# Kernel optimization log

Hardware: AMD Instinct MI355X
Metric: run time of the kernel (lower is better)

The kernel has to match this reference:

```python
import jax, jax.numpy as jnp
import numpy as np

V, D, H, HR, E, C = 32000, 512, 2048, 512, 8, 16
B, S = 2048, 128
MAX_PATH_LEN = 5
MAX_VISITS = 1
NEG = -1e9


def setup_inputs() -> dict:
    key = jax.random.key(0)
    ks = jax.random.split(key, 16)
    sc = 0.02
    emb = jax.random.normal(ks[0], (V, D), jnp.float32) * sc
    emb = emb.at[0].set(0.0)  # padding_idx = 0
    inp = {
        'input_ids': jax.random.randint(ks[1], (B, S), 0, V, jnp.int32),
        'emb': emb,
        'rW1': jax.random.normal(ks[2], (D, HR), jnp.float32) * sc,
        'rb1': jnp.zeros((HR,), jnp.float32),
        'rW2': jax.random.normal(ks[3], (HR, E + 1), jnp.float32) * sc,
        'rb2': jnp.zeros((E + 1,), jnp.float32),
        'eW1': jax.random.normal(ks[4], (E, D, H), jnp.float32) * sc,
        'eb1': jnp.zeros((E, H), jnp.float32),
        'eW2': jax.random.normal(ks[5], (E, H, D), jnp.float32) * sc,
        'eb2': jnp.zeros((E, D), jnp.float32),
        'etag': jax.random.normal(ks[6], (E, D), jnp.float32) * 0.1,  # specialization_tag
        'cW': jax.random.normal(ks[7], (D, C), jnp.float32) * sc,
        'cb': jnp.zeros((C,), jnp.float32),
    }
    return inp


def _goe_forward(input_ids, emb, rW1, rb1, rW2, rb2, eW1, eb1, eW2, eb2, etag, cW, cb):
    # mean-pooled token embeddings -> [B, D]
    rep = emb[input_ids].mean(axis=1)
    b = rep.shape[0]
    active = jnp.ones((b,), bool)
    visits = jnp.zeros((b, E), jnp.int32)
    final = jnp.zeros_like(rep)
    total_ent = jnp.asarray(0.0, rep.dtype)

    for _ in range(MAX_PATH_LEN):
        # router with visit-count masking
        hr = jax.nn.relu(rep @ rW1 + rb1)
        logits = hr @ rW2 + rb2  # [B, E+1]
        mask = jnp.concatenate([visits >= MAX_VISITS,
                                jnp.zeros((b, 1), bool)], axis=1)
        logits = jnp.where(mask, NEG, logits)
        probs = jax.nn.softmax(logits, axis=1)
        ent_per = -(probs * jnp.log(probs + 1e-9)).sum(axis=1)
        n_act = active.sum()
        step_ent = jnp.where(active, ent_per, 0.0).sum() / jnp.maximum(n_act, 1)
        total_ent = total_ent + jnp.where(n_act > 0, step_ent, 0.0)

        # eval-mode hard argmax decision (index E == terminate)
        decision = jnp.argmax(logits, axis=1)
        terminate = decision == E
        newly_term = active & terminate
        final = jnp.where(newly_term[:, None], rep, final)
        continuing = active & ~terminate
        chosen = jnp.clip(decision, 0, E - 1)

        # dense all-expert MLP, then gather the chosen expert's output
        hh = jax.nn.relu(jnp.einsum('bd,edh->beh', rep, eW1) + eb1)  # [B,E,H]
        out = jnp.einsum('beh,ehd->bed', hh, eW2) + eb2 + etag       # [B,E,D]
        new_rep = jnp.take_along_axis(out, chosen[:, None, None], axis=1)[:, 0, :]

        rep = jnp.where(continuing[:, None], new_rep, rep)
        visits = visits + jax.nn.one_hot(chosen, E, dtype=visits.dtype) \
            * continuing[:, None].astype(visits.dtype)
        active = continuing

    # samples still active after max_path_len keep their current representation
    final = jnp.where(active[:, None], rep, final)
    class_logits = final @ cW + cb
    return class_logits, total_ent


def reference(input_ids, emb, rW1, rb1, rW2, rb2, eW1, eb1, eW2, eb2, etag, cW, cb):
    return _goe_forward(input_ids, emb, rW1, rb1, rW2, rb2, eW1, eb1, eW2, eb2, etag, cW, cb)
```

## Files before the change

kernel.cpp:

```cpp
#include <hip/hip_runtime.h>
#include <cstdint>

#define BB 2048
#define SS 128
#define DD 512
#define HHID 2048
#define HRR 512
#define EE 8
#define CC 16
#define LSTEPS 5
#define MAXROWS 3072
#define NBLK128 24

typedef __bf16 bf16_t;
typedef __bf16 bf16x8 __attribute__((ext_vector_type(8)));
typedef float  f32x4  __attribute__((ext_vector_type(4)));

#define AS1 __attribute__((address_space(1)))
#define AS3 __attribute__((address_space(3)))

__device__ __forceinline__ void gload16(void* lds, const void* g){
  __builtin_amdgcn_global_load_lds((const AS1 uint32_t*)g, (AS3 uint32_t*)lds, 16, 0, 0);
}

__device__ __forceinline__ void split2(float v, bf16_t* h, bf16_t* l){
  bf16_t hh = (bf16_t)v;
  *h = hh;
  *l = (bf16_t)(v - (float)hh);
}

__global__ __launch_bounds__(256) void init_k(int* active, int* visits, int* cont,
                                              int* counts, double* total){
  int i = blockIdx.x*256 + threadIdx.x;
  if (i < BB){ active[i]=1; visits[i]=0; cont[i]=-1; }
  if (blockIdx.x == 0 && threadIdx.x < EE) counts[threadIdx.x]=0;
  if (i == 0) *total = 0.0;
}

__global__ __launch_bounds__(256) void tsplit_k(const float* __restrict__ W,
                                                bf16_t* __restrict__ Th,
                                                bf16_t* __restrict__ Tl,
                                                int K, int N){
  const size_t slice = (size_t)blockIdx.z * (size_t)K * (size_t)N;
  const float* Ws = W + slice;
  bf16_t* Ths = Th + slice;
  bf16_t* Tls = Tl + slice;
  __shared__ float tile[64][65];
  const int n0 = blockIdx.x*64, k0 = blockIdx.y*64;
  const int tx = threadIdx.x & 63, ty = threadIdx.x >> 6;
  #pragma unroll
  for (int i=0;i<16;++i){
    int kk = (i<<2) + ty;
    tile[kk][tx] = Ws[(size_t)(k0+kk)*N + n0 + tx];
  }
  __syncthreads();
  #pragma unroll
  for (int i=0;i<16;++i){
    int nn = (i<<2) + ty;
    float v = tile[tx][nn];
    size_t o = (size_t)(n0+nn)*K + k0 + tx;
    bf16_t h = (bf16_t)v;
    Ths[o] = h;
    Tls[o] = (bf16_t)(v - (float)h);
  }
}

__global__ __launch_bounds__(256) void pool_k(const int* __restrict__ ids,
                                              const float* __restrict__ emb,
                                              float* __restrict__ rep,
                                              bf16_t* __restrict__ rhi,
                                              bf16_t* __restrict__ rlo){
  __shared__ int sid[SS];
  __shared__ double red[128][4];
  const int b = blockIdx.x, t = threadIdx.x;
  if (t < SS) sid[t] = ids[b*SS + t];
  __syncthreads();
  const int half = t >> 7;
  const int c4   = t & 127;
  double a[4] = {0.0,0.0,0.0,0.0};
  for (int s = half; s < SS; s += 16){
    float4 v[8];
    #pragma unroll
    for (int u=0;u<8;++u)
      v[u] = *(const float4*)(emb + (size_t)sid[s + 2*u]*DD + (c4<<2));
    #pragma unroll
    for (int u=0;u<8;++u){
      a[0]+=(double)v[u].x; a[1]+=(double)v[u].y;
      a[2]+=(double)v[u].z; a[3]+=(double)v[u].w;
    }
  }
  if (half){
    red[c4][0]=a[0]; red[c4][1]=a[1]; red[c4][2]=a[2]; red[c4][3]=a[3];
  }
  __syncthreads();
  if (!half){
    float vv[4];
    #pragma unroll
    for (int j=0;j<4;++j) vv[j] = (float)((a[j] + red[c4][j]) * (1.0/SS));
    size_t o = (size_t)b*DD + (c4<<2);
    *(float4*)(rep + o) = make_float4(vv[0],vv[1],vv[2],vv[3]);
    #pragma unroll
    for (int j=0;j<4;++j) split2(vv[j], &rhi[o+j], &rlo[o+j]);
  }
}

__global__ __launch_bounds__(256, 2) void e1gemm_k(
    const bf16_t* __restrict__ Agh, const bf16_t* __restrict__ Agl,
    const bf16_t* __restrict__ Wgh, const bf16_t* __restrict__ Wgl,
    const float* __restrict__ bias,
    bf16_t* __restrict__ Ohi, bf16_t* __restrict__ Olo,
    const bf16_t* __restrict__ zrow,
    const int* __restrict__ list, const int* __restrict__ blkexp)
{
  constexpr int K = DD;
  constexpr int N = HHID;
  const int e = blkexp[blockIdx.y];
  if (e < 0) return;
  const int m0 = blockIdx.y * 128;
  const int n0 = blockIdx.x * 128;
  const bf16_t* Wh = Wgh + (size_t)e*(size_t)N*(size_t)K;
  const bf16_t* Wl = Wgl + (size_t)e*(size_t)N*(size_t)K;
  const float*  be = bias + (size_t)e*N;

  __shared__ __align__(16) bf16_t Ah[2][128*32], Al[2][128*32];
  __shared__ __align__(16) bf16_t Bh[2][128*32], Bl[2][128*32];
  __shared__ int sGi[128];

  const int t = threadIdx.x;
  const int L = t & 63, w = t >> 6;
  const int wm = w >> 1, wn = w & 1;

  if (t < 128) sGi[t] = list[m0 + t];
  __syncthreads();

  const int rIn = L >> 2;
// ... 54 lines not shown
      bvh[ni] = *(const bf16x8*)((const char*)Bh[cur] + off);
      bvl[ni] = *(const bf16x8*)((const char*)Bl[cur] + off);
    }
    #pragma unroll
    for (int mi=0;mi<4;++mi)
      #pragma unroll
      for (int ni=0;ni<4;++ni){
        acc[mi][ni] = __builtin_amdgcn_mfma_f32_16x16x32_bf16(avh[mi], bvh[ni], acc[mi][ni], 0,0,0);
        acc[mi][ni] = __builtin_amdgcn_mfma_f32_16x16x32_bf16(avh[mi], bvl[ni], acc[mi][ni], 0,0,0);
        acc[mi][ni] = __builtin_amdgcn_mfma_f32_16x16x32_bf16(avl[mi], bvh[ni], acc[mi][ni], 0,0,0);
      }
    __syncthreads();
    cur ^= 1;
  }

  const int cL = L & 15, rL4 = (L>>4)<<2;
  #pragma unroll
  for (int mi=0;mi<4;++mi){
    #pragma unroll
    for (int ni=0;ni<4;++ni){
      const int col = n0 + wn*64 + ni*16 + cL;
      const float bv = be[col];
      #pragma unroll
      for (int r=0;r<4;++r){
        const int trow = wm*64 + mi*16 + rL4 + r;
        float val = fmaxf(acc[mi][ni][r] + bv, 0.f);
        size_t o = (size_t)(m0+trow)*(size_t)N + col;
        split2(val, &Ohi[o], &Olo[o]);
      }
    }
  }
}

template<int BM, int BN, bool RELU, bool EXPERT, bool GATHER, bool SCATTER, bool EXTRA, bool SPLITOUT>
__global__ __launch_bounds__(256, 2) void mgemm_k(
    const bf16_t* __restrict__ Agh, const bf16_t* __restrict__ Agl,
    const bf16_t* __restrict__ Wgh, const bf16_t* __restrict__ Wgl,
    const float* __restrict__ bias, const float* __restrict__ extra,
    float* __restrict__ Of, bf16_t* __restrict__ Ohi, bf16_t* __restrict__ Olo,
    float* __restrict__ repf, bf16_t* __restrict__ rhi, bf16_t* __restrict__ rlo,
    const bf16_t* __restrict__ zrow,
    const int* __restrict__ list, const int* __restrict__ blkexp,
    int K, int N)
{
  int e = 0;
  if constexpr (EXPERT){ e = blkexp[(blockIdx.y*BM)>>7]; if (e < 0) return; }
  const int m0 = blockIdx.y*BM;
  const int n0 = blockIdx.x*BN;
  const bf16_t* Wh = Wgh + (EXPERT ? (size_t)e*(size_t)N*(size_t)K : 0);
  const bf16_t* Wl = Wgl + (EXPERT ? (size_t)e*(size_t)N*(size_t)K : 0);
  const float*  be = bias + (EXPERT ? (size_t)e*N : 0);
  const float*  xe = EXTRA ? (extra + (size_t)e*(size_t)N) : nullptr;

  __shared__ __align__(16) bf16_t Ah[2][BM*64], Al[2][BM*64];
  __shared__ __align__(16) bf16_t Bh[2][BN*64], Bl[2][BN*64];
  __shared__ int sGi[BM];

  const int t = threadIdx.x;
  const int L = t & 63, w = t >> 6;

  constexpr int MI = BM/32;
  constexpr int NI = BN/32;
  const int wm = w >> 1;
  const int wn = w & 1;

  constexpr int AQ = BM/8;
  constexpr int BQ = BN/8;
  const int rS = L>>3, sS = L&7;
  const int ss = sS ^ rS;

  if constexpr (GATHER || SCATTER){
    if (t < BM) sGi[t] = list[m0 + t];
  }
  if constexpr (GATHER) __syncthreads();

  auto stage = [&](int k0, int bb){
    if (w < 2){
      const bf16_t* gb = (w==0) ? Agh : Agl;
      bf16_t* sb = (w==0) ? Ah[bb] : Al[bb];
      #pragma unroll
      for (int i=0;i<AQ;++i){
        int r = i*8 + rS;
        const bf16_t* src;
        if constexpr (GATHER){
          int gi = sGi[r];
          src = (gi >= 0) ? (gb + (size_t)gi*K + k0 + ss*8) : (zrow + ss*8);
        } else {
          src = gb + (size_t)(m0+r)*K + k0 + ss*8;
        }
        gload16((char*)sb + i*1024, src);
      }
    } else {
      const bf16_t* gb = (w==2) ? Wh : Wl;
      bf16_t* sb = (w==2) ? Bh[bb] : Bl[bb];
      #pragma unroll
      for (int i=0;i<BQ;++i){
        int r = i*8 + rS;
        gload16((char*)sb + i*1024, gb + (size_t)(n0+r)*K + k0 + ss*8);
      }
    }
  };

  f32x4 acc[MI][NI];
  #pragma unroll
  for (int i=0;i<MI;++i)
    #pragma unroll
    for (int j=0;j<NI;++j){ f32x4 z = {0.f,0.f,0.f,0.f}; acc[i][j]=z; }

  stage(0, 0);
  __syncthreads();

  const int NT = K >> 6;
  int cur = 0;
  for (int tk = 0; tk < NT; ++tk){
    if (tk + 1 < NT) stage((tk+1) << 6, cur ^ 1);

    #pragma unroll
    for (int kk=0; kk<2; ++kk){
      const int g = (kk<<2) + (L>>4);
      bf16x8 avh[MI], avl[MI];
      #pragma unroll
      for (int mi=0;mi<MI;++mi){
        int row = wm*(BM/2) + mi*16 + (L&15);
        int off = row*128 + ((g ^ (row&7))<<4);
        avh[mi] = *(const bf16x8*)((const char*)Ah[cur] + off);
        avl[mi] = *(const bf16x8*)((const char*)Al[cur] + off);
      }
      bf16x8 bvh[NI], bvl[NI];
      #pragma unroll
      for (int ni=0;ni<NI;++ni){
        int row = wn*(BN/2) + ni*16 + (L&15);
        int off = row*128 + ((g ^ (row&7))<<4);
        bvh[ni] = *(const bf16x8*)((const char*)Bh[cur] + off);
        bvl[ni] = *(const bf16x8*)((const char*)Bl[cur] + off);
      }
      #pragma unroll
      for (int mi=0;mi<MI;++mi)
        #pragma unroll
        for (int ni=0;ni<NI;++ni){
          acc[mi][ni] = __builtin_amdgcn_mfma_f32_16x16x32_bf16(avh[mi], bvh[ni], acc[mi][ni], 0,0,0);
          acc[mi][ni] = __builtin_amdgcn_mfma_f32_16x16x32_bf16(avh[mi], bvl[ni], acc[mi][ni], 0,0,0);
          acc[mi][ni] = __builtin_amdgcn_mfma_f32_16x16x32_bf16(avl[mi], bvh[ni], acc[mi][ni], 0,0,0);
        }
    }
    __syncthreads();
    cur ^= 1;
  }

  const int cL = L & 15, rL4 = (L>>4)<<2;
  #pragma unroll
  for (int mi=0;mi<MI;++mi){
    #pragma unroll
    for (int ni=0;ni<NI;++ni){
      const int col = n0 + wn*(BN/2) + ni*16 + cL;
      float bv = be[col];
      if constexpr (EXTRA) bv += xe[col];
      #pragma unroll
      for (int r=0;r<4;++r){
        const int trow = wm*(BM/2) + mi*16 + rL4 + r;
        float val = acc[mi][ni][r] + bv;
        if constexpr (RELU) val = fmaxf(val, 0.f);
        if constexpr (SCATTER){
          int orow = sGi[trow];
          if (orow >= 0){
            size_t o = (size_t)orow*DD + col;
            repf[o] = val;
            split2(val, &rhi[o], &rlo[o]);
          }
        } else if constexpr (SPLITOUT){
          size_t o = (size_t)(m0+trow)*(size_t)N + col;
          split2(val, &Ohi[o], &Olo[o]);
        } else {
          Of[(size_t)(m0+trow)*(size_t)N + col] = val;
        }
      }
    }
  }
}

__global__ __launch_bounds__(256) void decide_k(
    const float* __restrict__ hr, const float* __restrict__ rW2, const float* __restrict__ rb2,
    const float* __restrict__ rep, float* __restrict__ final_,
    float* __restrict__ ent, int* __restrict__ wasact,
    int* __restrict__ active, int* __restrict__ visits,
    int* __restrict__ cont, int* __restrict__ counts)
{
  __shared__ float srw2[HRR*9];
  const int t = threadIdx.x;
  for (int i = t; i < HRR*9; i += 256) srw2[i] = rW2[i];
  __syncthreads();

  const int w = t >> 6, lane = t & 63;
  const int b = blockIdx.x*4 + w;
  if (!active[b]){
    if (lane == 0){ ent[b]=0.f; wasact[b]=0; cont[b]=-1; }
    return;
  }
  const float* h = hr + (size_t)b*HRR;
  float p[9];
  #pragma unroll
  for (int j=0;j<9;++j) p[j]=0.f;
  for (int k=lane; k<HRR; k+=64){
    const float hv = h[k];
    const float* wr = srw2 + k*9;
    #pragma unroll
    for (int j=0;j<9;++j) p[j] = fmaf(hv, wr[j], p[j]);
  }
  #pragma unroll
  for (int off=32; off>=1; off>>=1){
    #pragma unroll
    for (int j=0;j<9;++j) p[j] += __shfl_xor(p[j], off, 64);
  }
  bool term = false;
  if (lane == 0){
    const int vis = visits[b];
    float lg[9];
    #pragma unroll
    for (int j=0;j<9;++j) lg[j] = p[j] + rb2[j];
    #pragma unroll
    for (int j=0;j<EE;++j) if ((vis>>j)&1) lg[j] = -1e9f;
    float m = lg[0];
    #pragma unroll
    for (int j=1;j<9;++j) m = fmaxf(m, lg[j]);
    float ex[9]; float s = 0.f;
    #pragma unroll
    for (int j=0;j<9;++j){ ex[j]=expf(lg[j]-m); s+=ex[j]; }
    float ev = 0.f;
    #pragma unroll
    for (int j=0;j<9;++j){ float pr=ex[j]/s; ev -= pr*logf(pr+1e-9f); }
    ent[b]=ev; wasact[b]=1;
    int arg=0; float best=lg[0];
    #pragma unroll
    for (int j=1;j<9;++j) if (lg[j]>best){ best=lg[j]; arg=j; }
    if (arg == EE){
      cont[b]=-1; active[b]=0; term=true;
    } else {
      cont[b]=arg; visits[b]=vis|(1<<arg);
      atomicAdd(&counts[arg],1);
    }
  }
  if (__shfl(term ? 1 : 0, 0, 64)){
    const float* rp = rep   + (size_t)b*DD;
    float*       fp = final_+ (size_t)b*DD;
    for (int d=lane; d<DD; d+=64) fp[d]=rp[d];
  }
}

__global__ __launch_bounds__(256) void reduce_scatter_k(
    const float* __restrict__ ent, const int* __restrict__ wasact,
    const int* __restrict__ cont,
    int* __restrict__ counts, int* __restrict__ blkexp, int* __restrict__ list,
    double* __restrict__ total)
{
  const int t = threadIdx.x;
  double s = 0.0; int c = 0;
  for (int i=t;i<BB;i+=256){ s += (double)ent[i]; c += wasact[i]; }
  __shared__ double sd[256];
  __shared__ int    si[256];
  sd[t]=s; si[t]=c;
  __syncthreads();
  for (int off=128; off>=1; off>>=1){
    if (t < off){ sd[t]+=sd[t+off]; si[t]+=si[t+off]; }
    __syncthreads();
  }
  __shared__ int so[9]; __shared__ int sc[8]; __shared__ int scur[8];
  if (t == 0){
    if (si[0] > 0) *total += sd[0] / (double)si[0];
    int off = 0;
    for (int e2=0;e2<EE;++e2){
      so[e2]=off; sc[e2]=counts[e2]; scur[e2]=0;
      off += (counts[e2] + 127) & ~127;
    }
    so[8]=off;
    for (int r=0;r<NBLK128;++r){
      int ee=-1;
      for (int e2=0;e2<EE;++e2)
        if (r*128 >= so[e2] && (r+1)*128 <= so[e2+1]) ee=e2;
      blkexp[r]=ee;
    }
  }
  __syncthreads();
  for (int e2=0;e2<EE;++e2){
    for (int s2=so[e2]+sc[e2]+t; s2<so[e2+1]; s2+=256) list[s2]=-1;
  }
  for (int i=t;i<BB;i+=256){
    int e2 = cont[i];
    if (e2 >= 0){
      int p2 = atomicAdd(&scur[e2], 1);
      list[so[e2] + p2] = i;
    }
  }
  if (t < EE) counts[t]=0;
}

__global__ __launch_bounds__(256) void cls_k(const float* __restrict__ rep,
    const float* __restrict__ final_, const int* __restrict__ active,
    const float* __restrict__ cW, const float* __restrict__ cb,
    const double* __restrict__ total, float* __restrict__ out)
{
  __shared__ float scw[DD*CC];
  const int t = threadIdx.x;
  for (int i = t; i < DD*CC; i += 256) scw[i] = cW[i];
  __syncthreads();

  const int w = t >> 6, lane = t & 63;
  const int b = blockIdx.x*4 + w;
  if (b == 0 && lane == 0) out[BB*CC] = (float)(*total);
  const float* src = active[b] ? rep + (size_t)b*DD : final_ + (size_t)b*DD;
  float c[CC];
  #pragma unroll
  for (int j=0;j<CC;++j) c[j]=0.f;
  for (int k=lane;k<DD;k+=64){
    float v = src[k];
    const float* wr = scw + k*CC;
    #pragma unroll
    for (int j=0;j<CC;++j) c[j] = fmaf(v, wr[j], c[j]);
  }
  #pragma unroll
  for (int off=32;off>=1;off>>=1){
    #pragma unroll
    for (int j=0;j<CC;++j) c[j] += __shfl_xor(c[j], off, 64);
  }
  if (lane == 0){
    float* op = out + (size_t)b*CC;
    #pragma unroll
// ... 1 lines not shown
  }
}

extern "C" void kernel_launch(void* const* d_in, const int* in_sizes, int n_in,
                              void* d_out, int out_size, void* d_ws, size_t ws_size,
                              hipStream_t stream)
{
  const int*   ids = (const int*)  d_in[0];
  const float* emb = (const float*)d_in[1];
  const float* rW1 = (const float*)d_in[2];
  const float* rb1 = (const float*)d_in[3];
  const float* rW2 = (const float*)d_in[4];
  const float* rb2 = (const float*)d_in[5];
  const float* eW1 = (const float*)d_in[6];
  const float* eb1 = (const float*)d_in[7];
  const float* eW2 = (const float*)d_in[8];
  const float* eb2 = (const float*)d_in[9];
  const float* etag= (const float*)d_in[10];
  const float* cW  = (const float*)d_in[11];
  const float* cb  = (const float*)d_in[12];
  float* out = (float*)d_out;

  char* p = (char*)d_ws;
  auto alloc = [&](size_t bytes)->char*{
    char* r = p; p += (bytes + 255) & ~(size_t)255; return r;
  };
  float*  rep    = (float*) alloc((size_t)BB*DD*4);
  float*  hr     = (float*) alloc((size_t)BB*HRR*4);
  float*  final_ = (float*) alloc((size_t)BB*DD*4);
  bf16_t* rep_hi = (bf16_t*)alloc((size_t)BB*DD*2);
  bf16_t* rep_lo = (bf16_t*)alloc((size_t)BB*DD*2);
  bf16_t* hh_hi  = (bf16_t*)alloc((size_t)MAXROWS*HHID*2);
  bf16_t* hh_lo  = (bf16_t*)alloc((size_t)MAXROWS*HHID*2);
  bf16_t* rW1t_h = (bf16_t*)alloc((size_t)DD*HRR*2);
  bf16_t* rW1t_l = (bf16_t*)alloc((size_t)DD*HRR*2);
  bf16_t* eW1t_h = (bf16_t*)alloc((size_t)EE*DD*HHID*2);
  bf16_t* eW1t_l = (bf16_t*)alloc((size_t)EE*DD*HHID*2);
  bf16_t* eW2t_h = (bf16_t*)alloc((size_t)EE*DD*HHID*2);
  bf16_t* eW2t_l = (bf16_t*)alloc((size_t)EE*DD*HHID*2);
  bf16_t* zrow   = (bf16_t*)alloc(4096);
  float*  ent    = (float*) alloc((size_t)BB*4);
  int* wasact = (int*)alloc((size_t)BB*4);
  int* cont   = (int*)alloc((size_t)BB*4);
  int* active = (int*)alloc((size_t)BB*4);
  int* visits = (int*)alloc((size_t)BB*4);
  int* list   = (int*)alloc((size_t)MAXROWS*4);
  int* counts = (int*)alloc(64);
  int* blkexp = (int*)alloc(NBLK128*4);
  double* total = (double*)alloc(16);

  hipMemsetAsync(final_, 0, (size_t)BB*DD*4, stream);
  hipMemsetAsync(zrow, 0, 4096, stream);
  init_k<<<BB/256, 256, 0, stream>>>(active, visits, cont, counts, total);

  tsplit_k<<<dim3(HRR/64, DD/64, 1), 256, 0, stream>>>(rW1, rW1t_h, rW1t_l, DD, HRR);
  tsplit_k<<<dim3(HHID/64, DD/64, EE), 256, 0, stream>>>(eW1, eW1t_h, eW1t_l, DD, HHID);
  tsplit_k<<<dim3(DD/64, HHID/64, EE), 256, 0, stream>>>(eW2, eW2t_h, eW2t_l, HHID, DD);

  pool_k<<<BB, 256, 0, stream>>>(ids, emb, rep, rep_hi, rep_lo);

  for (int step=0; step<LSTEPS; ++step){
    mgemm_k<64,64, true,false,false,false,false,false><<<dim3(HRR/64, BB/64), 256, 0, stream>>>(
        rep_hi, rep_lo, rW1t_h, rW1t_l, rb1, nullptr,
        hr, nullptr, nullptr, nullptr, nullptr, nullptr,
        zrow, nullptr, nullptr, DD, HRR);

    decide_k<<<BB/4, 256, 0, stream>>>(hr, rW2, rb2, rep, final_, ent, wasact,
                                       active, visits, cont, counts);
    reduce_scatter_k<<<1, 256, 0, stream>>>(ent, wasact, cont, counts, blkexp, list, total);

    e1gemm_k<<<dim3(HHID/128, NBLK128), 256, 0, stream>>>(
        rep_hi, rep_lo, eW1t_h, eW1t_l, eb1, hh_hi, hh_lo, zrow, list, blkexp);

    mgemm_k<64,64, false,true,false,true,true,false><<<dim3(DD/64, MAXROWS/64), 256, 0, stream>>>(
        hh_hi, hh_lo, eW2t_h, eW2t_l, eb2, etag,
        nullptr, nullptr, nullptr, rep, rep_hi, rep_lo,
        zrow, list, blkexp, HHID, DD);
  }

  cls_k<<<BB/4, 256, 0, stream>>>(rep, final_, active, cW, cb, total, out);
}
```

Measured before the change: 602.3 us.

## Triple-buffer mgemm with K=32 stages and fuse scatter into decide kernel

The split-bf16 MFMA GEMM drops from double-buffered 64-wide K tiles to triple-buffered 32-wide K tiles. It uses explicit vmcnt waits and raw barriers so that two loads stay in flight while the current tile is computed, with a new swizzle matched to the narrower rows. The separate single-block reduce_scatter kernel is folded into decide_k using a last-block-done atomic counter, which removes one launch per step. The unused GATHER and SPLITOUT template paths are also removed. This adds risk from the hand-written waitcnt counts and the grid-wide counter pattern.

```diff
diff --git a/kernel.cpp b/kernel.cpp
--- a/kernel.cpp
+++ b/kernel.cpp
@@ -30,11 +30,11 @@
 }
 
 __global__ __launch_bounds__(256) void init_k(int* active, int* visits, int* cont,
-                                              int* counts, double* total){
+                                              int* counts, int* done, double* total){
   int i = blockIdx.x*256 + threadIdx.x;
   if (i < BB){ active[i]=1; visits[i]=0; cont[i]=-1; }
   if (blockIdx.x == 0 && threadIdx.x < EE) counts[threadIdx.x]=0;
-  if (i == 0) *total = 0.0;
+  if (i == 0){ *total = 0.0; *done = 0; }
 }
 
 __global__ __launch_bounds__(256) void tsplit_k(const float* __restrict__ W,
@@ -221,14 +221,13 @@
   }
 }
 
-template<int BM, int BN, bool RELU, bool EXPERT, bool GATHER, bool SCATTER, bool EXTRA, bool SPLITOUT>
+template<int BM, int BN, bool RELU, bool EXPERT, bool SCATTER, bool EXTRA>
 __global__ __launch_bounds__(256, 2) void mgemm_k(
     const bf16_t* __restrict__ Agh, const bf16_t* __restrict__ Agl,
     const bf16_t* __restrict__ Wgh, const bf16_t* __restrict__ Wgl,
     const float* __restrict__ bias, const float* __restrict__ extra,
-    float* __restrict__ Of, bf16_t* __restrict__ Ohi, bf16_t* __restrict__ Olo,
+    float* __restrict__ Of,
     float* __restrict__ repf, bf16_t* __restrict__ rhi, bf16_t* __restrict__ rlo,
-    const bf16_t* __restrict__ zrow,
     const int* __restrict__ list, const int* __restrict__ blkexp,
     int K, int N)
 {
@@ -241,8 +240,8 @@
   const float*  be = bias + (EXPERT ? (size_t)e*N : 0);
   const float*  xe = EXTRA ? (extra + (size_t)e*(size_t)N) : nullptr;
 
-  __shared__ __align__(16) bf16_t Ah[2][BM*64], Al[2][BM*64];
-  __shared__ __align__(16) bf16_t Bh[2][BN*64], Bl[2][BN*64];
+  __shared__ __align__(16) bf16_t Ah[3][BM*32], Al[3][BM*32];
+  __shared__ __align__(16) bf16_t Bh[3][BN*32], Bl[3][BN*32];
   __shared__ int sGi[BM];
 
   const int t = threadIdx.x;
@@ -253,39 +252,31 @@
   const int wm = w >> 1;
   const int wn = w & 1;
 
-  constexpr int AQ = BM/8;
-  constexpr int BQ = BN/8;
-  const int rS = L>>3, sS = L&7;
-  const int ss = sS ^ rS;
-
-  if constexpr (GATHER || SCATTER){
+  if constexpr (SCATTER){
     if (t < BM) sGi[t] = list[m0 + t];
   }
-  if constexpr (GATHER) __syncthreads();
+
+  const int rIn = L >> 2;
+  const int pSl = L & 3;
 
   auto stage = [&](int k0, int bb){
     if (w < 2){
       const bf16_t* gb = (w==0) ? Agh : Agl;
       bf16_t* sb = (w==0) ? Ah[bb] : Al[bb];
       #pragma unroll
-      for (int i=0;i<AQ;++i){
-        int r = i*8 + rS;
-        const bf16_t* src;
-        if constexpr (GATHER){
-          int gi = sGi[r];
-          src = (gi >= 0) ? (gb + (size_t)gi*K + k0 + ss*8) : (zrow + ss*8);
-        } else {
-          src = gb + (size_t)(m0+r)*K + k0 + ss*8;
-        }
-        gload16((char*)sb + i*1024, src);
+      for (int i=0;i<BM/16;++i){
+        int r  = i*16 + rIn;
+        int cs = pSl ^ ((r>>1)&3);
+        gload16((char*)sb + i*1024, gb + (size_t)(m0+r)*K + k0 + cs*8);
       }
     } else {
       const bf16_t* gb = (w==2) ? Wh : Wl;
       bf16_t* sb = (w==2) ? Bh[bb] : Bl[bb];
       #pragma unroll
-      for (int i=0;i<BQ;++i){
-        int r = i*8 + rS;
-        gload16((char*)sb + i*1024, gb + (size_t)(n0+r)*K + k0 + ss*8);
+      for (int i=0;i<BN/16;++i){
+        int r  = i*16 + rIn;
+        int cs = pSl ^ ((r>>1)&3);
+        gload16((char*)sb + i*1024, gb + (size_t)(n0+r)*K + k0 + cs*8);
       }
     }
   };
@@ -296,44 +287,46 @@
     #pragma unroll
     for (int j=0;j<NI;++j){ f32x4 z = {0.f,0.f,0.f,0.f}; acc[i][j]=z; }
 
+  const int NT = K >> 5;
   stage(0, 0);
-  __syncthreads();
-
-  const int NT = K >> 6;
-  int cur = 0;
+  if (NT > 1) stage(32, 1);
+
+  const int g = L >> 4;
   for (int tk = 0; tk < NT; ++tk){
-    if (tk + 1 < NT) stage((tk+1) << 6, cur ^ 1);
-
-    #pragma unroll
-    for (int kk=0; kk<2; ++kk){
-      const int g = (kk<<2) + (L>>4);
-      bf16x8 avh[MI], avl[MI];
-      #pragma unroll
-      for (int mi=0;mi<MI;++mi){
-        int row = wm*(BM/2) + mi*16 + (L&15);
-        int off = row*128 + ((g ^ (row&7))<<4);
-        avh[mi] = *(const bf16x8*)((const char*)Ah[cur] + off);
-        avl[mi] = *(const bf16x8*)((const char*)Al[cur] + off);
-      }
-      bf16x8 bvh[NI], bvl[NI];
+    if (tk + 2 < NT) stage((tk+2) << 5, (tk+2)%3);
+    const int nf = ((tk+1 < NT) ? 1 : 0) + ((tk+2 < NT) ? 1 : 0);
+    if (nf == 2)      asm volatile("s_waitcnt vmcnt(8)" ::: "memory");
+    else if (nf == 1) asm volatile("s_waitcnt vmcnt(4)" ::: "memory");
+    else              asm volatile("s_waitcnt vmcnt(0)" ::: "memory");
+    __builtin_amdgcn_s_barrier();
+    __builtin_amdgcn_sched_barrier(0);
+
+    const int cur = tk % 3;
+    bf16x8 avh[MI], avl[MI], bvh[NI], bvl[NI];
+    #pragma unroll
+    for (int mi=0;mi<MI;++mi){
+      int row = wm*(BM/2) + mi*16 + (L&15);
+      int off = row*64 + ((g ^ ((row>>1)&3))<<4);
+      avh[mi] = *(const bf16x8*)((const char*)Ah[cur] + off);
+      avl[mi] = *(const bf16x8*)((const char*)Al[cur] + off);
+    }
+    #pragma unroll
+    for (int ni=0;ni<NI;++ni){
+      int row = wn*(BN/2) + ni*16 + (L&15);
+      int off = row*64 + ((g ^ ((row>>1)&3))<<4);
+      bvh[ni] = *(const bf16x8*)((const char*)Bh[cur] + off);
+      bvl[ni] = *(const bf16x8*)((const char*)Bl[cur] + off);
+    }
+    #pragma unroll
+    for (int mi=0;mi<MI;++mi)
       #pragma unroll
       for (int ni=0;ni<NI;++ni){
-        int row = wn*(BN/2) + ni*16 + (L&15);
-        int off = row*128 + ((g ^ (row&7))<<4);
-        bvh[ni] = *(const bf16x8*)((const char*)Bh[cur] + off);
-        bvl[ni] = *(const bf16x8*)((const char*)Bl[cur] + off);
-      }
-      #pragma unroll
-      for (int mi=0;mi<MI;++mi)
-        #pragma unroll
-        for (int ni=0;ni<NI;++ni){
-          acc[mi][ni] = __builtin_amdgcn_mfma_f32_16x16x32_bf16(avh[mi], bvh[ni], acc[mi][ni], 0,0,0);
-          acc[mi][ni] = __builtin_amdgcn_mfma_f32_16x16x32_bf16(avh[mi], bvl[ni], acc[mi][ni], 0,0,0);
-          acc[mi][ni] = __builtin_amdgcn_mfma_f32_16x16x32_bf16(avl[mi], bvh[ni], acc[mi][ni], 0,0,0);
-        }
-    }
-    __syncthreads();
-    cur ^= 1;
+        acc[mi][ni] = __builtin_amdgcn_mfma_f32_16x16x32_bf16(avh[mi], bvh[ni], acc[mi][ni], 0,0,0);
+        acc[mi][ni] = __builtin_amdgcn_mfma_f32_16x16x32_bf16(avh[mi], bvl[ni], acc[mi][ni], 0,0,0);
+        acc[mi][ni] = __builtin_amdgcn_mfma_f32_16x16x32_bf16(avl[mi], bvh[ni], acc[mi][ni], 0,0,0);
+      }
+    __builtin_amdgcn_sched_barrier(0);
+    __builtin_amdgcn_s_barrier();
   }
 
   const int cL = L & 15, rL4 = (L>>4)<<2;
@@ -356,9 +349,6 @@
             repf[o] = val;
             split2(val, &rhi[o], &rlo[o]);
           }
-        } else if constexpr (SPLITOUT){
-          size_t o = (size_t)(m0+trow)*(size_t)N + col;
-          split2(val, &Ohi[o], &Olo[o]);
         } else {
           Of[(size_t)(m0+trow)*(size_t)N + col] = val;
         }
@@ -372,7 +362,9 @@
     const float* __restrict__ rep, float* __restrict__ final_,
     float* __restrict__ ent, int* __restrict__ wasact,
     int* __restrict__ active, int* __restrict__ visits,
-    int* __restrict__ cont, int* __restrict__ counts)
+    int* __restrict__ cont, int* __restrict__ counts,
+    int* __restrict__ done, int* __restrict__ blkexp, int* __restrict__ list,
+    double* __restrict__ total)
 {
   __shared__ float srw2[HRR*9];
   const int t = threadIdx.x;
@@ -381,72 +373,76 @@
 
   const int w = t >> 6, lane = t & 63;
   const int b = blockIdx.x*4 + w;
-  if (!active[b]){
+  const bool act = active[b] != 0;
+  if (!act){
     if (lane == 0){ ent[b]=0.f; wasact[b]=0; cont[b]=-1; }
-    return;
-  }
-  const float* h = hr + (size_t)b*HRR;
-  float p[9];
-  #pragma unroll
-  for (int j=0;j<9;++j) p[j]=0.f;
-  for (int k=lane; k<HRR; k+=64){
-    const float hv = h[k];
-    const float* wr = srw2 + k*9;
-    #pragma unroll
-    for (int j=0;j<9;++j) p[j] = fmaf(hv, wr[j], p[j]);
-  }
-  #pragma unroll
-  for (int off=32; off>=1; off>>=1){
-    #pragma unroll
-    for (int j=0;j<9;++j) p[j] += __shfl_xor(p[j], off, 64);
-  }
-  bool term = false;
-  if (lane == 0){
-    const int vis = visits[b];
-    float lg[9];
-    #pragma unroll
-    for (int j=0;j<9;++j) lg[j] = p[j] + rb2[j];
-    #pragma unroll
-    for (int j=0;j<EE;++j) if ((vis>>j)&1) lg[j] = -1e9f;
-    float m = lg[0];
-    #pragma unroll
-    for (int j=1;j<9;++j) m = fmaxf(m, lg[j]);
-    float ex[9]; float s = 0.f;
-    #pragma unroll
-    for (int j=0;j<9;++j){ ex[j]=expf(lg[j]-m); s+=ex[j]; }
-    float ev = 0.f;
-    #pragma unroll
-    for (int j=0;j<9;++j){ float pr=ex[j]/s; ev -= pr*logf(pr+1e-9f); }
-    ent[b]=ev; wasact[b]=1;
-    int arg=0; float best=lg[0];
-    #pragma unroll
-    for (int j=1;j<9;++j) if (lg[j]>best){ best=lg[j]; arg=j; }
-    if (arg == EE){
-      cont[b]=-1; active[b]=0; term=true;
-    } else {
-      cont[b]=arg; visits[b]=vis|(1<<arg);
-      atomicAdd(&counts[arg],1);
-    }
-  }
-  if (__shfl(term ? 1 : 0, 0, 64)){
-    const float* rp = rep   + (size_t)b*DD;
-    float*       fp = final_+ (size_t)b*DD;
-    for (int d=lane; d<DD; d+=64) fp[d]=rp[d];
-  }
-}
-
-__global__ __launch_bounds__(256) void reduce_scatter_k(
-    const float* __restrict__ ent, const int* __restrict__ wasact,
-    const int* __restrict__ cont,
-    int* __restrict__ counts, int* __restrict__ blkexp, int* __restrict__ list,
-    double* __restrict__ total)
-{
-  const int t = threadIdx.x;
-  double s = 0.0; int c = 0;
-  for (int i=t;i<BB;i+=256){ s += (double)ent[i]; c += wasact[i]; }
+  } else {
+    const float* h = hr + (size_t)b*HRR;
+    float p[9];
+    #pragma unroll
+    for (int j=0;j<9;++j) p[j]=0.f;
+    for (int k=lane; k<HRR; k+=64){
+      const float hv = h[k];
+      const float* wr = srw2 + k*9;
+      #pragma unroll
+      for (int j=0;j<9;++j) p[j] = fmaf(hv, wr[j], p[j]);
+    }
+    #pragma unroll
+    for (int off=32; off>=1; off>>=1){
+      #pragma unroll
+      for (int j=0;j<9;++j) p[j] += __shfl_xor(p[j], off, 64);
+    }
+    bool term = false;
+    if (lane == 0){
+      const int vis = visits[b];
+      float lg[9];
+      #pragma unroll
+      for (int j=0;j<9;++j) lg[j] = p[j] + rb2[j];
+      #pragma unroll
+      for (int j=0;j<EE;++j) if ((vis>>j)&1) lg[j] = -1e9f;
+      float m = lg[0];
+      #pragma unroll
+      for (int j=1;j<9;++j) m = fmaxf(m, lg[j]);
+      float ex[9]; float s = 0.f;
+      #pragma unroll
+      for (int j=0;j<9;++j){ ex[j]=expf(lg[j]-m); s+=ex[j]; }
+      float ev = 0.f;
+      #pragma unroll
+      for (int j=0;j<9;++j){ float pr=ex[j]/s; ev -= pr*logf(pr+1e-9f); }
+      ent[b]=ev; wasact[b]=1;
+      int arg=0; float best=lg[0];
+      #pragma unroll
+      for (int j=1;j<9;++j) if (lg[j]>best){ best=lg[j]; arg=j; }
+      if (arg == EE){
+        cont[b]=-1; active[b]=0; term=true;
+      } else {
+        cont[b]=arg; visits[b]=vis|(1<<arg);
+        atomicAdd(&counts[arg],1);
+      }
+    }
+    if (__shfl(term ? 1 : 0, 0, 64)){
+      const float* rp = rep   + (size_t)b*DD;
+      float*       fp = final_+ (size_t)b*DD;
+      for (int d=lane; d<DD; d+=64) fp[d]=rp[d];
+    }
+  }
+  __syncthreads();
+
+  __shared__ int slast;
+  if (t == 0){
+    __threadfence();
+    int prev = atomicAdd(done, 1);
+    slast = (prev == (int)gridDim.x - 1) ? 1 : 0;
+  }
+  __syncthreads();
+  if (!slast) return;
+  __threadfence();
+
+  double s2 = 0.0; int c2 = 0;
+  for (int i=t;i<BB;i+=256){ s2 += (double)ent[i]; c2 += wasact[i]; }
   __shared__ double sd[256];
   __shared__ int    si[256];
-  sd[t]=s; si[t]=c;
+  sd[t]=s2; si[t]=c2;
   __syncthreads();
   for (int off=128; off>=1; off>>=1){
     if (t < off){ sd[t]+=sd[t+off]; si[t]+=si[t+off]; }
@@ -470,7 +466,7 @@
   }
   __syncthreads();
   for (int e2=0;e2<EE;++e2){
-    for (int s2=so[e2]+sc[e2]+t; s2<so[e2+1]; s2+=256) list[s2]=-1;
+    for (int s3=so[e2]+sc[e2]+t; s3<so[e2+1]; s3+=256) list[s3]=-1;
   }
   for (int i=t;i<BB;i+=256){
     int e2 = cont[i];
@@ -480,6 +476,8 @@
     }
   }
   if (t < EE) counts[t]=0;
+  __syncthreads();
+  if (t == 0) *done = 0;
 }
 
 __global__ __launch_bounds__(256) void cls_k(const float* __restrict__ rep,
@@ -562,11 +560,12 @@
   int* list   = (int*)alloc((size_t)MAXROWS*4);
   int* counts = (int*)alloc(64);
   int* blkexp = (int*)alloc(NBLK128*4);
+  int* done   = (int*)alloc(64);
   double* total = (double*)alloc(16);
 
   hipMemsetAsync(final_, 0, (size_t)BB*DD*4, stream);
   hipMemsetAsync(zrow, 0, 4096, stream);
-  init_k<<<BB/256, 256, 0, stream>>>(active, visits, cont, counts, total);
+  init_k<<<BB/256, 256, 0, stream>>>(active, visits, cont, counts, done, total);
 
   tsplit_k<<<dim3(HRR/64, DD/64, 1), 256, 0, stream>>>(rW1, rW1t_h, rW1t_l, DD, HRR);
   tsplit_k<<<dim3(HHID/64, DD/64, EE), 256, 0, stream>>>(eW1, eW1t_h, eW1t_l, DD, HHID);
@@ -575,22 +574,20 @@
   pool_k<<<BB, 256, 0, stream>>>(ids, emb, rep, rep_hi, rep_lo);
 
   for (int step=0; step<LSTEPS; ++step){
-    mgemm_k<64,64, true,false,false,false,false,false><<<dim3(HRR/64, BB/64), 256, 0, stream>>>(
+    mgemm_k<64,64, true,false,false,false><<<dim3(HRR/64, BB/64), 256, 0, stream>>>(
         rep_hi, rep_lo, rW1t_h, rW1t_l, rb1, nullptr,
-        hr, nullptr, nullptr, nullptr, nullptr, nullptr,
-        zrow, nullptr, nullptr, DD, HRR);
+        hr, nullptr, nullptr, nullptr, nullptr, nullptr, DD, HRR);
 
     decide_k<<<BB/4, 256, 0, stream>>>(hr, rW2, rb2, rep, final_, ent, wasact,
-                                       active, visits, cont, counts);
-    reduce_scatter_k<<<1, 256, 0, stream>>>(ent, wasact, cont, counts, blkexp, list, total);
+                                       active, visits, cont, counts,
+                                       done, blkexp, list, total);
 
     e1gemm_k<<<dim3(HHID/128, NBLK128), 256, 0, stream>>>(
         rep_hi, rep_lo, eW1t_h, eW1t_l, eb1, hh_hi, hh_lo, zrow, list, blkexp);
 
-    mgemm_k<64,64, false,true,false,true,true,false><<<dim3(DD/64, MAXROWS/64), 256, 0, stream>>>(
+    mgemm_k<64,64, false,true,true,true><<<dim3(DD/64, MAXROWS/64), 256, 0, stream>>>(
         hh_hi, hh_lo, eW2t_h, eW2t_l, eb2, etag,
-        nullptr, nullptr, nullptr, rep, rep_hi, rep_lo,
-        zrow, list, blkexp, HHID, DD);
+        nullptr, rep, rep_hi, rep_lo, list, blkexp, HHID, DD);
   }
 
   cls_k<<<BB/4, 256, 0, stream>>>(rep, final_, active, cW, cb, total, out);
```

Result: slower. 1.107 ms (+83.8%).

## Split-K the expert down-projection, merge setup kernels, specialize router GEMM

Applied to the files above, without the earlier changes.

The second expert GEMM (K=2048) now runs as a two-way split-K over a z grid dimension. It writes fp32 partials, and a new finalize kernel sums them, adds bias and tag, and scatters into rep and its hi/lo split. The pooling and three weight transpose-split kernels are merged into one launch, and the router GEMM becomes a fixed-shape kernel. The aim is more blocks for the low-occupancy down-projection and fewer launches. The cost is an extra partial-buffer round trip through memory and one extra kernel per step.

```diff
diff --git a/kernel.cpp b/kernel.cpp
--- a/kernel.cpp
+++ b/kernel.cpp
@@ -37,27 +37,26 @@
   if (i == 0) *total = 0.0;
 }
 
-__global__ __launch_bounds__(256) void tsplit_k(const float* __restrict__ W,
-                                                bf16_t* __restrict__ Th,
-                                                bf16_t* __restrict__ Tl,
-                                                int K, int N){
-  const size_t slice = (size_t)blockIdx.z * (size_t)K * (size_t)N;
+__device__ __forceinline__ void tsplit_body(float* tile , int t,
+    const float* __restrict__ W, bf16_t* __restrict__ Th, bf16_t* __restrict__ Tl,
+    int K, int N, int bx, int by, int bz)
+{
+  const size_t slice = (size_t)bz*(size_t)K*(size_t)N;
   const float* Ws = W + slice;
   bf16_t* Ths = Th + slice;
   bf16_t* Tls = Tl + slice;
-  __shared__ float tile[64][65];
-  const int n0 = blockIdx.x*64, k0 = blockIdx.y*64;
-  const int tx = threadIdx.x & 63, ty = threadIdx.x >> 6;
+  const int n0 = bx*64, k0 = by*64;
+  const int tx = t & 63, ty = t >> 6;
   #pragma unroll
   for (int i=0;i<16;++i){
     int kk = (i<<2) + ty;
-    tile[kk][tx] = Ws[(size_t)(k0+kk)*N + n0 + tx];
+    tile[kk*65 + tx] = Ws[(size_t)(k0+kk)*N + n0 + tx];
   }
   __syncthreads();
   #pragma unroll
   for (int i=0;i<16;++i){
     int nn = (i<<2) + ty;
-    float v = tile[tx][nn];
+    float v = tile[tx*65 + nn];
     size_t o = (size_t)(n0+nn)*K + k0 + tx;
     bf16_t h = (bf16_t)v;
     Ths[o] = h;
@@ -65,42 +64,60 @@
   }
 }
 
-__global__ __launch_bounds__(256) void pool_k(const int* __restrict__ ids,
-                                              const float* __restrict__ emb,
-                                              float* __restrict__ rep,
-                                              bf16_t* __restrict__ rhi,
-                                              bf16_t* __restrict__ rlo){
-  __shared__ int sid[SS];
-  __shared__ double red[128][4];
-  const int b = blockIdx.x, t = threadIdx.x;
-  if (t < SS) sid[t] = ids[b*SS + t];
-  __syncthreads();
-  const int half = t >> 7;
-  const int c4   = t & 127;
-  double a[4] = {0.0,0.0,0.0,0.0};
-  for (int s = half; s < SS; s += 16){
-    float4 v[8];
-    #pragma unroll
-    for (int u=0;u<8;++u)
-      v[u] = *(const float4*)(emb + (size_t)sid[s + 2*u]*DD + (c4<<2));
-    #pragma unroll
-    for (int u=0;u<8;++u){
-      a[0]+=(double)v[u].x; a[1]+=(double)v[u].y;
-      a[2]+=(double)v[u].z; a[3]+=(double)v[u].w;
-    }
-  }
-  if (half){
-    red[c4][0]=a[0]; red[c4][1]=a[1]; red[c4][2]=a[2]; red[c4][3]=a[3];
-  }
-  __syncthreads();
-  if (!half){
-    float vv[4];
-    #pragma unroll
-    for (int j=0;j<4;++j) vv[j] = (float)((a[j] + red[c4][j]) * (1.0/SS));
-    size_t o = (size_t)b*DD + (c4<<2);
-    *(float4*)(rep + o) = make_float4(vv[0],vv[1],vv[2],vv[3]);
-    #pragma unroll
-    for (int j=0;j<4;++j) split2(vv[j], &rhi[o+j], &rlo[o+j]);
+__global__ __launch_bounds__(256) void setup_k(
+    const int* __restrict__ ids, const float* __restrict__ emb,
+    float* __restrict__ rep, bf16_t* __restrict__ rhi, bf16_t* __restrict__ rlo,
+    const float* __restrict__ rW1, bf16_t* __restrict__ rW1t_h, bf16_t* __restrict__ rW1t_l,
+    const float* __restrict__ eW1, bf16_t* __restrict__ eW1t_h, bf16_t* __restrict__ eW1t_l,
+    const float* __restrict__ eW2, bf16_t* __restrict__ eW2t_h, bf16_t* __restrict__ eW2t_l)
+{
+  __shared__ __align__(16) char smem[16640];
+  const int bid = blockIdx.x, t = threadIdx.x;
+  if (bid < BB){
+    int* sid = (int*)smem;
+    double* red = (double*)(smem + 512);
+    const int b = bid;
+    if (t < SS) sid[t] = ids[b*SS + t];
+    __syncthreads();
+    const int half = t >> 7;
+    const int c4   = t & 127;
+    double a[4] = {0.0,0.0,0.0,0.0};
+    for (int s = half; s < SS; s += 16){
+      float4 v[8];
+      #pragma unroll
+      for (int u=0;u<8;++u)
+        v[u] = *(const float4*)(emb + (size_t)sid[s + 2*u]*DD + (c4<<2));
+      #pragma unroll
+      for (int u=0;u<8;++u){
+        a[0]+=(double)v[u].x; a[1]+=(double)v[u].y;
+        a[2]+=(double)v[u].z; a[3]+=(double)v[u].w;
+      }
+    }
+    if (half){
+      #pragma unroll
+      for (int j=0;j<4;++j) red[c4*4+j] = a[j];
+    }
+    __syncthreads();
+    if (!half){
+      float vv[4];
+      #pragma unroll
+      for (int j=0;j<4;++j) vv[j] = (float)((a[j] + red[c4*4+j]) * (1.0/SS));
+      size_t o = (size_t)b*DD + (c4<<2);
+      *(float4*)(rep + o) = make_float4(vv[0],vv[1],vv[2],vv[3]);
+      #pragma unroll
+      for (int j=0;j<4;++j) split2(vv[j], &rhi[o+j], &rlo[o+j]);
+    }
+  } else if (bid < BB + 64){
+    int r = bid - BB;
+    tsplit_body((float*)smem, t, rW1, rW1t_h, rW1t_l, DD, HRR, r & 7, r >> 3, 0);
+  } else if (bid < BB + 64 + 2048){
+    int r = bid - BB - 64;
+    int z = r >> 8, rem = r & 255;
+    tsplit_body((float*)smem, t, eW1, eW1t_h, eW1t_l, DD, HHID, rem & 31, rem >> 5, z);
+  } else {
+    int r = bid - BB - 64 - 2048;
+    int z = r >> 8, rem = r & 255;
+    tsplit_body((float*)smem, t, eW2, eW2t_h, eW2t_l, HHID, DD, rem & 7, rem >> 3, z);
   }
 }
 
@@ -221,80 +238,50 @@
   }
 }
 
-template<int BM, int BN, bool RELU, bool EXPERT, bool GATHER, bool SCATTER, bool EXTRA, bool SPLITOUT>
-__global__ __launch_bounds__(256, 2) void mgemm_k(
+__global__ __launch_bounds__(256, 2) void rgemm_k(
     const bf16_t* __restrict__ Agh, const bf16_t* __restrict__ Agl,
     const bf16_t* __restrict__ Wgh, const bf16_t* __restrict__ Wgl,
-    const float* __restrict__ bias, const float* __restrict__ extra,
-    float* __restrict__ Of, bf16_t* __restrict__ Ohi, bf16_t* __restrict__ Olo,
-    float* __restrict__ repf, bf16_t* __restrict__ rhi, bf16_t* __restrict__ rlo,
-    const bf16_t* __restrict__ zrow,
-    const int* __restrict__ list, const int* __restrict__ blkexp,
-    int K, int N)
-{
-  int e = 0;
-  if constexpr (EXPERT){ e = blkexp[(blockIdx.y*BM)>>7]; if (e < 0) return; }
+    const float* __restrict__ bias, float* __restrict__ Of)
+{
+  constexpr int K = DD, N = HRR, BM = 64, BN = 64;
   const int m0 = blockIdx.y*BM;
   const int n0 = blockIdx.x*BN;
-  const bf16_t* Wh = Wgh + (EXPERT ? (size_t)e*(size_t)N*(size_t)K : 0);
-  const bf16_t* Wl = Wgl + (EXPERT ? (size_t)e*(size_t)N*(size_t)K : 0);
-  const float*  be = bias + (EXPERT ? (size_t)e*N : 0);
-  const float*  xe = EXTRA ? (extra + (size_t)e*(size_t)N) : nullptr;
 
   __shared__ __align__(16) bf16_t Ah[2][BM*64], Al[2][BM*64];
   __shared__ __align__(16) bf16_t Bh[2][BN*64], Bl[2][BN*64];
-  __shared__ int sGi[BM];
 
   const int t = threadIdx.x;
   const int L = t & 63, w = t >> 6;
-
-  constexpr int MI = BM/32;
-  constexpr int NI = BN/32;
-  const int wm = w >> 1;
-  const int wn = w & 1;
-
-  constexpr int AQ = BM/8;
-  constexpr int BQ = BN/8;
+  const int wm = w >> 1, wn = w & 1;
+
   const int rS = L>>3, sS = L&7;
   const int ss = sS ^ rS;
-
-  if constexpr (GATHER || SCATTER){
-    if (t < BM) sGi[t] = list[m0 + t];
-  }
-  if constexpr (GATHER) __syncthreads();
 
   auto stage = [&](int k0, int bb){
     if (w < 2){
       const bf16_t* gb = (w==0) ? Agh : Agl;
       bf16_t* sb = (w==0) ? Ah[bb] : Al[bb];
       #pragma unroll
-      for (int i=0;i<AQ;++i){
+      for (int i=0;i<8;++i){
         int r = i*8 + rS;
-        const bf16_t* src;
-        if constexpr (GATHER){
-          int gi = sGi[r];
-          src = (gi >= 0) ? (gb + (size_t)gi*K + k0 + ss*8) : (zrow + ss*8);
-        } else {
-          src = gb + (size_t)(m0+r)*K + k0 + ss*8;
-        }
-        gload16((char*)sb + i*1024, src);
+        gload16((char*)sb + i*1024, gb + (size_t)(m0+r)*K + k0 + ss*8);
       }
     } else {
-      const bf16_t* gb = (w==2) ? Wh : Wl;
+      const bf16_t* gb = (w==2) ? Wgh : Wgl;
       bf16_t* sb = (w==2) ? Bh[bb] : Bl[bb];
       #pragma unroll
-      for (int i=0;i<BQ;++i){
+      for (int i=0;i<8;++i){
         int r = i*8 + rS;
         gload16((char*)sb + i*1024, gb + (size_t)(n0+r)*K + k0 + ss*8);
       }
     }
   };
 
-  f32x4 acc[MI][NI];
-  #pragma unroll
-  for (int i=0;i<MI;++i)
-    #pragma unroll
-    for (int j=0;j<NI;++j){ f32x4 z = {0.f,0.f,0.f,0.f}; acc[i][j]=z; }
+  f32x4 acc[2][2];
+  #pragma unroll
+  for (int i=0;i<2;++i)
+    #pragma unroll
+    for (int j=0;j<2;++j){ f32x4 z = {0.f,0.f,0.f,0.f}; acc[i][j]=z; }
 
   stage(0, 0);
   __syncthreads();
@@ -303,30 +290,28 @@
   int cur = 0;
   for (int tk = 0; tk < NT; ++tk){
     if (tk + 1 < NT) stage((tk+1) << 6, cur ^ 1);
-
     #pragma unroll
     for (int kk=0; kk<2; ++kk){
       const int g = (kk<<2) + (L>>4);
-      bf16x8 avh[MI], avl[MI];
-      #pragma unroll
-      for (int mi=0;mi<MI;++mi){
-        int row = wm*(BM/2) + mi*16 + (L&15);
+      bf16x8 avh[2], avl[2], bvh[2], bvl[2];
+      #pragma unroll
+      for (int mi=0;mi<2;++mi){
+        int row = wm*32 + mi*16 + (L&15);
         int off = row*128 + ((g ^ (row&7))<<4);
         avh[mi] = *(const bf16x8*)((const char*)Ah[cur] + off);
         avl[mi] = *(const bf16x8*)((const char*)Al[cur] + off);
       }
-      bf16x8 bvh[NI], bvl[NI];
-      #pragma unroll
-      for (int ni=0;ni<NI;++ni){
-        int row = wn*(BN/2) + ni*16 + (L&15);
+      #pragma unroll
+      for (int ni=0;ni<2;++ni){
+        int row = wn*32 + ni*16 + (L&15);
         int off = row*128 + ((g ^ (row&7))<<4);
         bvh[ni] = *(const bf16x8*)((const char*)Bh[cur] + off);
         bvl[ni] = *(const bf16x8*)((const char*)Bl[cur] + off);
       }
       #pragma unroll
-      for (int mi=0;mi<MI;++mi)
+      for (int mi=0;mi<2;++mi)
         #pragma unroll
-        for (int ni=0;ni<NI;++ni){
+        for (int ni=0;ni<2;++ni){
           acc[mi][ni] = __builtin_amdgcn_mfma_f32_16x16x32_bf16(avh[mi], bvh[ni], acc[mi][ni], 0,0,0);
           acc[mi][ni] = __builtin_amdgcn_mfma_f32_16x16x32_bf16(avh[mi], bvl[ni], acc[mi][ni], 0,0,0);
           acc[mi][ni] = __builtin_amdgcn_mfma_f32_16x16x32_bf16(avl[mi], bvh[ni], acc[mi][ni], 0,0,0);
@@ -338,32 +323,156 @@
 
   const int cL = L & 15, rL4 = (L>>4)<<2;
   #pragma unroll
-  for (int mi=0;mi<MI;++mi){
-    #pragma unroll
-    for (int ni=0;ni<NI;++ni){
-      const int col = n0 + wn*(BN/2) + ni*16 + cL;
-      float bv = be[col];
-      if constexpr (EXTRA) bv += xe[col];
+  for (int mi=0;mi<2;++mi){
+    #pragma unroll
+    for (int ni=0;ni<2;++ni){
+      const int col = n0 + wn*32 + ni*16 + cL;
+      const float bv = bias[col];
       #pragma unroll
       for (int r=0;r<4;++r){
-        const int trow = wm*(BM/2) + mi*16 + rL4 + r;
-        float val = acc[mi][ni][r] + bv;
-        if constexpr (RELU) val = fmaxf(val, 0.f);
-        if constexpr (SCATTER){
-          int orow = sGi[trow];
-          if (orow >= 0){
-            size_t o = (size_t)orow*DD + col;
-            repf[o] = val;
-            split2(val, &rhi[o], &rlo[o]);
-          }
-        } else if constexpr (SPLITOUT){
-          size_t o = (size_t)(m0+trow)*(size_t)N + col;
-          split2(val, &Ohi[o], &Olo[o]);
-        } else {
-          Of[(size_t)(m0+trow)*(size_t)N + col] = val;
+        const int trow = wm*32 + mi*16 + rL4 + r;
+        Of[(size_t)(m0+trow)*(size_t)N + col] = fmaxf(acc[mi][ni][r] + bv, 0.f);
+      }
+    }
+  }
+}
+
+__global__ __launch_bounds__(256, 2) void e2gemm_k(
+    const bf16_t* __restrict__ Agh, const bf16_t* __restrict__ Agl,
+    const bf16_t* __restrict__ Wgh, const bf16_t* __restrict__ Wgl,
+    float* __restrict__ Cpart, const int* __restrict__ blkexp)
+{
+  constexpr int K = HHID, N = DD, BM = 64, BN = 64, KS = K/2;
+  const int e = blkexp[(blockIdx.y*BM)>>7];
+  if (e < 0) return;
+  const int m0 = blockIdx.y*BM;
+  const int n0 = blockIdx.x*BN;
+  const int kbase = blockIdx.z * KS;
+  const bf16_t* Wh = Wgh + (size_t)e*(size_t)N*(size_t)K;
+  const bf16_t* Wl = Wgl + (size_t)e*(size_t)N*(size_t)K;
+  float* Cp = Cpart + (size_t)blockIdx.z*MAXROWS*DD;
+
+  __shared__ __align__(16) bf16_t Ah[2][BM*64], Al[2][BM*64];
+  __shared__ __align__(16) bf16_t Bh[2][BN*64], Bl[2][BN*64];
+
+  const int t = threadIdx.x;
+  const int L = t & 63, w = t >> 6;
+  const int wm = w >> 1, wn = w & 1;
+
+  const int rS = L>>3, sS = L&7;
+  const int ss = sS ^ rS;
+
+  auto stage = [&](int k0, int bb){
+    if (w < 2){
+      const bf16_t* gb = (w==0) ? Agh : Agl;
+      bf16_t* sb = (w==0) ? Ah[bb] : Al[bb];
+      #pragma unroll
+      for (int i=0;i<8;++i){
+        int r = i*8 + rS;
+        gload16((char*)sb + i*1024, gb + (size_t)(m0+r)*K + kbase + k0 + ss*8);
+      }
+    } else {
+      const bf16_t* gb = (w==2) ? Wh : Wl;
+      bf16_t* sb = (w==2) ? Bh[bb] : Bl[bb];
+      #pragma unroll
+      for (int i=0;i<8;++i){
+        int r = i*8 + rS;
+        gload16((char*)sb + i*1024, gb + (size_t)(n0+r)*K + kbase + k0 + ss*8);
+      }
+    }
+  };
+
+  f32x4 acc[2][2];
+  #pragma unroll
+  for (int i=0;i<2;++i)
+    #pragma unroll
+    for (int j=0;j<2;++j){ f32x4 z = {0.f,0.f,0.f,0.f}; acc[i][j]=z; }
+
+  stage(0, 0);
+  __syncthreads();
+
+  const int NT = KS >> 6;
+  int cur = 0;
+  for (int tk = 0; tk < NT; ++tk){
+    if (tk + 1 < NT) stage((tk+1) << 6, cur ^ 1);
+    #pragma unroll
+    for (int kk=0; kk<2; ++kk){
+      const int g = (kk<<2) + (L>>4);
+      bf16x8 avh[2], avl[2], bvh[2], bvl[2];
+      #pragma unroll
+      for (int mi=0;mi<2;++mi){
+        int row = wm*32 + mi*16 + (L&15);
+        int off = row*128 + ((g ^ (row&7))<<4);
+        avh[mi] = *(const bf16x8*)((const char*)Ah[cur] + off);
+        avl[mi] = *(const bf16x8*)((const char*)Al[cur] + off);
+      }
+      #pragma unroll
+      for (int ni=0;ni<2;++ni){
+        int row = wn*32 + ni*16 + (L&15);
+        int off = row*128 + ((g ^ (row&7))<<4);
+        bvh[ni] = *(const bf16x8*)((const char*)Bh[cur] + off);
+        bvl[ni] = *(const bf16x8*)((const char*)Bl[cur] + off);
+      }
+      #pragma unroll
+      for (int mi=0;mi<2;++mi)
+        #pragma unroll
+        for (int ni=0;ni<2;++ni){
+          acc[mi][ni] = __builtin_amdgcn_mfma_f32_16x16x32_bf16(avh[mi], bvh[ni], acc[mi][ni], 0,0,0);
+          acc[mi][ni] = __builtin_amdgcn_mfma_f32_16x16x32_bf16(avh[mi], bvl[ni], acc[mi][ni], 0,0,0);
+          acc[mi][ni] = __builtin_amdgcn_mfma_f32_16x16x32_bf16(avl[mi], bvh[ni], acc[mi][ni], 0,0,0);
         }
-      }
-    }
+    }
+    __syncthreads();
+    cur ^= 1;
+  }
+
+  const int cL = L & 15, rL4 = (L>>4)<<2;
+  #pragma unroll
+  for (int mi=0;mi<2;++mi){
+    #pragma unroll
+    for (int ni=0;ni<2;++ni){
+      const int col = n0 + wn*32 + ni*16 + cL;
+      #pragma unroll
+      for (int r=0;r<4;++r){
+        const int trow = wm*32 + mi*16 + rL4 + r;
+        Cp[(size_t)(m0+trow)*(size_t)N + col] = acc[mi][ni][r];
+      }
+    }
+  }
+}
+
+__global__ __launch_bounds__(256) void e2fin_k(
+    const float* __restrict__ Cpart, const float* __restrict__ eb2,
+    const float* __restrict__ etag, const int* __restrict__ list,
+    const int* __restrict__ blkexp,
+    float* __restrict__ repf, bf16_t* __restrict__ rhi, bf16_t* __restrict__ rlo)
+{
+  const int m0 = blockIdx.x*64;
+  const int e = blkexp[m0>>7];
+  if (e < 0) return;
+  const float* bb = eb2 + (size_t)e*DD;
+  const float* xx = etag + (size_t)e*DD;
+  const int r = threadIdx.x >> 2;
+  const int cq = threadIdx.x & 3;
+  const int orow = list[m0 + r];
+  if (orow < 0) return;
+  const float* c0 = Cpart + (size_t)(m0+r)*DD;
+  const float* c1 = c0 + (size_t)MAXROWS*DD;
+  float* rf = repf + (size_t)orow*DD;
+  bf16_t* rh = rhi + (size_t)orow*DD;
+  bf16_t* rl = rlo + (size_t)orow*DD;
+  for (int c = cq*128; c < cq*128 + 128; c += 4){
+    float4 v0 = *(const float4*)(c0 + c);
+    float4 v1 = *(const float4*)(c1 + c);
+    float4 bv = *(const float4*)(bb + c);
+    float4 xv = *(const float4*)(xx + c);
+    float vals[4] = { v0.x + v1.x + bv.x + xv.x,
+                      v0.y + v1.y + bv.y + xv.y,
+                      v0.z + v1.z + bv.z + xv.z,
+                      v0.w + v1.w + bv.w + xv.w };
+    *(float4*)(rf + c) = make_float4(vals[0], vals[1], vals[2], vals[3]);
+    #pragma unroll
+    for (int j=0;j<4;++j) split2(vals[j], &rh[c+j], &rl[c+j]);
   }
 }
 
@@ -547,6 +656,7 @@
   bf16_t* rep_lo = (bf16_t*)alloc((size_t)BB*DD*2);
   bf16_t* hh_hi  = (bf16_t*)alloc((size_t)MAXROWS*HHID*2);
   bf16_t* hh_lo  = (bf16_t*)alloc((size_t)MAXROWS*HHID*2);
+  float*  Cpart  = (float*) alloc((size_t)2*MAXROWS*DD*4);
   bf16_t* rW1t_h = (bf16_t*)alloc((size_t)DD*HRR*2);
   bf16_t* rW1t_l = (bf16_t*)alloc((size_t)DD*HRR*2);
   bf16_t* eW1t_h = (bf16_t*)alloc((size_t)EE*DD*HHID*2);
@@ -568,17 +678,13 @@
   hipMemsetAsync(zrow, 0, 4096, stream);
   init_k<<<BB/256, 256, 0, stream>>>(active, visits, cont, counts, total);
 
-  tsplit_k<<<dim3(HRR/64, DD/64, 1), 256, 0, stream>>>(rW1, rW1t_h, rW1t_l, DD, HRR);
-  tsplit_k<<<dim3(HHID/64, DD/64, EE), 256, 0, stream>>>(eW1, eW1t_h, eW1t_l, DD, HHID);
-  tsplit_k<<<dim3(DD/64, HHID/64, EE), 256, 0, stream>>>(eW2, eW2t_h, eW2t_l, HHID, DD);
-
-  pool_k<<<BB, 256, 0, stream>>>(ids, emb, rep, rep_hi, rep_lo);
+  setup_k<<<BB + 64 + 2048 + 2048, 256, 0, stream>>>(
+      ids, emb, rep, rep_hi, rep_lo,
+      rW1, rW1t_h, rW1t_l, eW1, eW1t_h, eW1t_l, eW2, eW2t_h, eW2t_l);
 
   for (int step=0; step<LSTEPS; ++step){
-    mgemm_k<64,64, true,false,false,false,false,false><<<dim3(HRR/64, BB/64), 256, 0, stream>>>(
-        rep_hi, rep_lo, rW1t_h, rW1t_l, rb1, nullptr,
-        hr, nullptr, nullptr, nullptr, nullptr, nullptr,
-        zrow, nullptr, nullptr, DD, HRR);
+    rgemm_k<<<dim3(HRR/64, BB/64), 256, 0, stream>>>(
+        rep_hi, rep_lo, rW1t_h, rW1t_l, rb1, hr);
 
     decide_k<<<BB/4, 256, 0, stream>>>(hr, rW2, rb2, rep, final_, ent, wasact,
                                        active, visits, cont, counts);
@@ -587,10 +693,10 @@
     e1gemm_k<<<dim3(HHID/128, NBLK128), 256, 0, stream>>>(
         rep_hi, rep_lo, eW1t_h, eW1t_l, eb1, hh_hi, hh_lo, zrow, list, blkexp);
 
-    mgemm_k<64,64, false,true,false,true,true,false><<<dim3(DD/64, MAXROWS/64), 256, 0, stream>>>(
-        hh_hi, hh_lo, eW2t_h, eW2t_l, eb2, etag,
-        nullptr, nullptr, nullptr, rep, rep_hi, rep_lo,
-        zrow, list, blkexp, HHID, DD);
+    e2gemm_k<<<dim3(DD/64, MAXROWS/64, 2), 256, 0, stream>>>(
+        hh_hi, hh_lo, eW2t_h, eW2t_l, Cpart, blkexp);
+    e2fin_k<<<MAXROWS/64, 256, 0, stream>>>(
+        Cpart, eb2, etag, list, blkexp, rep, rep_hi, rep_lo);
   }
 
   cls_k<<<BB/4, 256, 0, stream>>>(rep, final_, active, cW, cb, total, out);
```

Measured after the change: 1.369 ms. +127.3%, slower.
